# Optimization experiments

Measured on AMD Instinct MI355X. Metric: run time of the kernel, lower is better.

The kernel has to match this reference:

```python
import jax, jax.numpy as jnp
import numpy as np

DIM = 256
N_EMBED = 16384
BETA = 0.25
FIX_LEN = 30.0  # fix_len_l2norm


def setup_inputs() -> dict:
    key = jax.random.key(0)
    k1, k2 = jax.random.split(key)
    z = jax.random.normal(k1, (16, DIM, 32, 32), dtype=jnp.float32)
    embedding = jax.random.normal(k2, (N_EMBED, DIM), dtype=jnp.float32)
    return {"z": z, "embedding": embedding}


def reference(z, embedding):
    # pre_len_l2norm: mean over (b,h,w) of the channel-dim L2 norm of z [b,c,h,w]
    pre_len = jnp.mean(jnp.linalg.norm(z, axis=1))
    zt = jnp.transpose(z, (0, 2, 3, 1))  # b h w c
    # use_l2_norm=False path: rescale only if pre_len >= fix_len_l2norm
    scale = jnp.where(pre_len >= FIX_LEN, FIX_LEN / pre_len, 1.0)
    zt = zt * scale

    z_flat = zt.reshape(-1, DIM)  # [N_tok, dim]
    # norm_type != 'rela_llm' -> scaled_ratio = fix_len_l2norm
    zs = jax.lax.stop_gradient(z_flat) / FIX_LEN
    # squared L2 distance: |z|^2 + |e|^2 - 2 z.e   -> [N_tok, n_embed]
    d = (jnp.sum(zs * zs, axis=1, keepdims=True)
         + jnp.sum(embedding * embedding, axis=1)
         - 2.0 * jnp.einsum('bd,nd->bn', zs, embedding))
    idx = jnp.argmin(d, axis=1)  # [N_tok]

    z_q = embedding[idx].reshape(zt.shape) * FIX_LEN  # gather + rescale
    diff = BETA * jnp.mean((jax.lax.stop_gradient(z_q) - zt) ** 2)
    z_q = zt + jax.lax.stop_gradient(z_q - zt)  # straight-through
    z_q = jnp.transpose(z_q, (0, 3, 1, 2))  # b c h w
    return z_q, diff, idx
```

## Files before the change

### kernel.cpp

```cpp
#include <hip/hip_runtime.h>
#include <hip/hip_fp16.h>
#include <math.h>

#define FIXLEN 30.0f
#define BETA   0.25f

typedef unsigned short u16;
typedef unsigned int   u32;
typedef unsigned long long u64;
typedef _Float16 half8 __attribute__((ext_vector_type(8)));
typedef float    f32x4 __attribute__((ext_vector_type(4)));

#define NRM_OFF    0
#define NRMX_OFF   256
#define CST_OFF    512
#define CNT_OFF    576
#define DIFF_OFF   1024
#define ZMAX_OFF   2048
#define EMAXL_OFF  6144
#define EMAXE_OFF  14336
#define E2_OFF     22528
#define BESTN_OFF  88064
#define PCNT_OFF   153600
#define PLIST_OFF  219136
#define CIDX_OFF   743424
#define CE2_OFF    808960
#define LIST2_OFF  874496
#define E2MIN_OFF  940032
#define ZS_OFF     1048576
#define ZH_OFF     1792000
#define EHC_OFF    10180608

__device__ inline void gl_lds16(const void* g, void* l) {
    __builtin_amdgcn_global_load_lds(
        (const __attribute__((address_space(1))) unsigned int*)g,
        (__attribute__((address_space(3))) unsigned int*)l, 16, 0, 0);
}

__global__ void k_split_e(const float* __restrict__ emb, float* __restrict__ e2,
                          float* __restrict__ emaxl, float* __restrict__ emaxe,
                          float* __restrict__ e2minp) {
    int gidx = blockIdx.x * 256 + threadIdx.x;
    int n = gidx >> 5;
    int c8 = (gidx & 31) * 8;
    const float* ep = emb + (size_t)n * 256 + c8;
    float4 v0 = *(const float4*)ep;
    float4 v1 = *(const float4*)(ep + 4);
    float vv[8] = {v0.x, v0.y, v0.z, v0.w, v1.x, v1.y, v1.z, v1.w};
    float s2 = 0.f, r2 = 0.f;
    #pragma unroll
    for (int k = 0; k < 8; ++k) {
        __half h = __float2half(vv[k]);
        float r = vv[k] - __half2float(h);
        s2 = fmaf(vv[k], vv[k], s2);
        r2 = fmaf(r, r, r2);
    }
    #pragma unroll
    for (int off = 16; off > 0; off >>= 1) {
        s2 += __shfl_down(s2, off, 32);
        r2 += __shfl_down(r2, off, 32);
    }
    __shared__ float L1[8], L2[8];
    if ((threadIdx.x & 31) == 0) {
        e2[n] = s2;
        L1[threadIdx.x >> 5] = r2;
        L2[threadIdx.x >> 5] = s2;
    }
    __syncthreads();
    if (threadIdx.x == 0) {
        float a = 0.f, bmax = 0.f, bmin = 3.4e38f;
        #pragma unroll
        for (int i = 0; i < 8; ++i) {
            a = fmaxf(a, L1[i]);
            bmax = fmaxf(bmax, L2[i]);
            bmin = fminf(bmin, L2[i]);
        }
        emaxl[blockIdx.x] = a;
        emaxe[blockIdx.x] = bmax;
        e2minp[blockIdx.x] = bmin;
    }
}

__global__ void k_split_z(const float* __restrict__ z, u16* __restrict__ zh,
                          float* __restrict__ zmax_part, float* __restrict__ zsumP) {
    int bi = blockIdx.x;
    int b = bi >> 6, rest = bi & 63;
    int c0 = (rest >> 4) * 64, s0 = (rest & 15) * 64;
    __shared__ float ld[64][65];
    __shared__ float red2[64][4];
    __shared__ float redz[64][4];
    __shared__ float rmax[64];
    int tid = threadIdx.x;
    #pragma unroll
    for (int p = 0; p < 16; ++p) {
        int idx = p * 256 + tid;
        int cc = idx >> 6, ss = idx & 63;
        ld[cc][ss] = z[(size_t)b * 262144 + (size_t)(c0 + cc) * 1024 + s0 + ss];
    }
    __syncthreads();
    int ss2 = tid >> 2, cq = tid & 3;
    int t = b * 1024 + s0 + ss2;
    float r2 = 0.f, zacc = 0.f;
    u32 pk[8];
    #pragma unroll
    for (int k = 0; k < 8; ++k) pk[k] = 0;
    #pragma unroll
    for (int j = 0; j < 16; ++j) {
        float raw = ld[cq * 16 + j][ss2];
        zacc = fmaf(raw, raw, zacc);
        float v = raw * (1.0f / 30.0f);
        __half h = __float2half(v);
        float vh = __half2float(h);
        float r = v - vh;
        r2 = fmaf(r, r, r2);
        __half hs = __float2half(-2.0f * vh);
        pk[j >> 1] |= ((u32)__half_as_ushort(hs)) << ((j & 1) * 16);
    }
    u16* dst = zh + (size_t)t * 256 + c0 + cq * 16;
    *(uint4*)dst = make_uint4(pk[0], pk[1], pk[2], pk[3]);
    *(uint4*)(dst + 8) = make_uint4(pk[4], pk[5], pk[6], pk[7]);
    red2[ss2][cq] = r2;
    redz[ss2][cq] = zacc;
    __syncthreads();
    if (tid < 64) {
        rmax[tid] = red2[tid][0] + red2[tid][1] + red2[tid][2] + red2[tid][3];
        zsumP[(size_t)(rest >> 4) * 16384 + b * 1024 + s0 + tid] =
            redz[tid][0] + redz[tid][1] + redz[tid][2] + redz[tid][3];
    }
    __syncthreads();
    for (int off = 32; off > 0; off >>= 1) {
        if (tid < off) rmax[tid] = fmaxf(rmax[tid], rmax[tid + off]);
        __syncthreads();
    }
    if (tid == 0) zmax_part[bi] = rmax[0];
}

__global__ void k_norm2(const float* __restrict__ zsumP, float* __restrict__ nrm_part,
                        float* __restrict__ nrmx_part) {
    int t = blockIdx.x * 256 + threadIdx.x;
    float tot = zsumP[t] + zsumP[16384 + t] + zsumP[32768 + t] + zsumP[49152 + t];
    float nrm = sqrtf(tot);
    __shared__ float rs[256], rm[256];
    rs[threadIdx.x] = nrm; rm[threadIdx.x] = nrm;
    __syncthreads();
    for (int off = 128; off > 0; off >>= 1) {
        if (threadIdx.x < off) {
            rs[threadIdx.x] += rs[threadIdx.x + off];
            rm[threadIdx.x] = fmaxf(rm[threadIdx.x], rm[threadIdx.x + off]);
        }
        __syncthreads();
    }
    if (threadIdx.x == 0) { nrm_part[blockIdx.x] = rs[0]; nrmx_part[blockIdx.x] = rm[0]; }
}

__global__ void k_scalars(const float* __restrict__ nrm_part, const float* __restrict__ nrmx_part,
                          const float* __restrict__ zmax_part, const float* __restrict__ emaxl,
                          const float* __restrict__ emaxe, const float* __restrict__ e2minp,
                          float* __restrict__ cst, int* __restrict__ cnt) {
    int tid = threadIdx.x;
    float s = (tid < 64) ? nrm_part[tid] : 0.f;
    float m = (tid < 64) ? nrmx_part[tid] : 0.f;
    float zm = 0.f, el = 0.f, ee = 0.f, em = 3.4e38f;
    for (int i = tid; i < 1024; i += 256) zm = fmaxf(zm, zmax_part[i]);
    for (int i = tid; i < 2048; i += 256) {
        el = fmaxf(el, emaxl[i]);
        ee = fmaxf(ee, emaxe[i]);
        em = fminf(em, e2minp[i]);
    }
    __shared__ float S[256], M[256], Z[256], L[256], E[256], Q[256];
    S[tid] = s; M[tid] = m; Z[tid] = zm; L[tid] = el; E[tid] = ee; Q[tid] = em;
    __syncthreads();
    for (int off = 128; off > 0; off >>= 1) {
        if (tid < off) {
            S[tid] += S[tid + off];
            M[tid] = fmaxf(M[tid], M[tid + off]);
            Z[tid] = fmaxf(Z[tid], Z[tid + off]);
            L[tid] = fmaxf(L[tid], L[tid + off]);
            E[tid] = fmaxf(E[tid], E[tid + off]);
            Q[tid] = fminf(Q[tid], Q[tid + off]);
        }
        __syncthreads();
    }
    if (tid == 0) {
        float pre_len = S[0] * (1.0f / 16384.0f);
        float scale = (pre_len >= FIXLEN) ? (FIXLEN / pre_len) : 1.0f;
        float inv_s = 1.0f / scale;
        cst[0] = scale;
        cst[1] = inv_s;
        cst[3] = M[0];
        float maxA  = M[0] * (1.0f / 30.0f);
        float maxEl = sqrtf(L[0]);
        float maxE  = sqrtf(E[0]);
        float maxZl = 2.0f * sqrtf(Z[0]);
        float eps = 2.0f * (maxA * maxEl + maxZl * maxE + maxZl * maxEl) + 0.03f;
        float EPS2 = 2.0f * eps;
        cst[2] = EPS2;
        float e2min = Q[0];
        float T = fmaf(2.0f * maxA, sqrtf(e2min), e2min * inv_s);
        cst[4] = T + 2.0f * EPS2 + 1.0f;
        cnt[0] = 0;
        cnt[1] = 0;
    }
}

__global__ void k_select(const float* __restrict__ e2, const float* __restrict__ cst,
                         int* __restrict__ candIdx, int* __restrict__ cnt) {
    int n = blockIdx.x * 256 + threadIdx.x;
    float inv_s = cst[1], maxA = cst[3] * (1.0f / 30.0f), Tc = cst[4];
    float v = e2[n];
    float lb = fmaf(-2.0f * maxA, sqrtf(v), v * inv_s);
    bool sel = lb <= Tc;
    u64 mask = __ballot(sel);
    if (mask) {
        int lane = threadIdx.x & 63;
        int leader = __ffsll((long long)mask) - 1;
        int base = 0;
        if (lane == leader) base = atomicAdd(cnt + 1, __popcll(mask));
        base = __shfl(base, leader);
        if (sel) {
            int rank = __popcll(mask & ((1ull << lane) - 1ull));
            candIdx[base + rank] = n;
        }
    }
}

__global__ void k_gather(const float* __restrict__ emb, const float* __restrict__ e2,
                         const float* __restrict__ cst, const int* __restrict__ cnt,
                         const int* __restrict__ candIdx, u16* __restrict__ ehc,
                         float* __restrict__ ce2) {
    int w = threadIdx.x >> 6, lane = threadIdx.x & 63;
    int wid = blockIdx.x * 4 + w;
    int C = cnt[1];
    int NP = (C + 255) & ~255;
    float inv_s = cst[1];
    for (int slot = wid; slot < NP; slot += 256) {
        if (slot < C) {
            int n = candIdx[slot];
            float4 v = *(const float4*)&emb[(size_t)n * 256 + lane * 4];
            u32 p0 = (u32)__half_as_ushort(__float2half(v.x)) |
                     ((u32)__half_as_ushort(__float2half(v.y)) << 16);
            u32 p1 = (u32)__half_as_ushort(__float2half(v.z)) |
                     ((u32)__half_as_ushort(__float2half(v.w)) << 16);
            *(uint2*)&ehc[(size_t)slot * 256 + lane * 4] = make_uint2(p0, p1);
            if (lane == 0) ce2[slot] = e2[n] * inv_s;
        } else {
            *(uint2*)&ehc[(size_t)slot * 256 + lane * 4] = make_uint2(0u, 0u);
            if (lane == 0) ce2[slot] = 3.0e37f;
        }
    }
}

__launch_bounds__(256, 2)
__global__ void k_cmfma(const u16* __restrict__ zh, const u16* __restrict__ ehc,
                        const float* __restrict__ ce2, const float* __restrict__ cst,
                        int* __restrict__ cnt, const int* __restrict__ candIdx,
                        int* __restrict__ pcnt, int* __restrict__ plist,
                        int* __restrict__ list2, int* __restrict__ bestn) {
    __shared__ __align__(16) char lds[51200];
    char* sAb = lds;
    char* sB0 = lds + 16384;
    char* sB1 = lds + 32768;
    float* d1buf  = (float*)(lds + 49152);
    float* limitS = (float*)(lds + 49664);
    int*   pcnts  = (int*)(lds + 49792);
    int*   pls    = (int*)(lds + 49920);

    int t0 = blockIdx.x * 32;
    int C = cnt[1];
    int nch = (C + 255) >> 8;
    float THR = cst[2] + 0.0625f;
    int tid = threadIdx.x, w = tid >> 6, lane = tid & 63;
    int ml = lane & 15, q = lane >> 4;
    int wn0 = w * 64;
    int x7 = ml & 7;
    int xb = (ml >> 1) & 3;
    int slB = q ^ xb;

    #pragma unroll
    for (int i = 0; i < 4; ++i) {
        int el = i * 256 + tid;
        int row = el >> 5, j = el & 31;
        int jsrc = (j & 24) | ((j & 7) ^ (row & 7));
        gl_lds16(zh + (size_t)(t0 + row) * 256 + jsrc * 8, sAb + el * 16);
    }
    #pragma unroll
    for (int i = 0; i < 4; ++i) {
        int el = i * 256 + tid;
        int row = el >> 2, j = el & 3;
        int jsrc = j ^ ((row >> 1) & 3);
        gl_lds16(ehc + (size_t)row * 256 + jsrc * 8, sB0 + el * 16);
    }

    float b1[8];
    #pragma unroll
    for (int k = 0; k < 8; ++k) b1[k] = 3.4e38f;

    #pragma unroll 1
    for (int c = 0; c < nch; ++c) {
        float etb[4];
        #pragma unroll
        for (int tj = 0; tj < 4; ++tj) etb[tj] = ce2[c * 256 + wn0 + tj * 16 + ml];
        f32x4 acc[2][4];
        #pragma unroll
        for (int ti = 0; ti < 2; ++ti)
            #pragma unroll
            for (int tj = 0; tj < 4; ++tj)
                acc[ti][tj] = (f32x4){etb[tj], etb[tj], etb[tj], etb[tj]};
        #pragma unroll
        for (int s = 0; s < 8; ++s) {
            __syncthreads();
            if (s < 7 || c + 1 < nch) {
                int s2 = (s + 1) & 7;
                int cc2 = (s == 7) ? (c + 1) : c;
                char* dst = (s & 1) ? sB0 : sB1;
                #pragma unroll
                for (int i = 0; i < 4; ++i) {
                    int el = i * 256 + tid;
                    int row = el >> 2, j = el & 3;
                    int jsrc = j ^ ((row >> 1) & 3);
                    gl_lds16(ehc + (size_t)(cc2 * 256 + row) * 256 + s2 * 32 + jsrc * 8,
                             dst + el * 16);
                }
            }
            __builtin_amdgcn_sched_barrier(0);
            const char* sB = (s & 1) ? sB1 : sB0;
            half8 A[2], B[4];
            #pragma unroll
            for (int tj = 0; tj < 4; ++tj)
                B[tj] = *(const half8*)(sB + (wn0 + tj * 16 + ml) * 64 + slB * 16);
            int slotA = (s >> 1) * 8 + ((((s & 1) * 4) + q) ^ x7);
            #pragma unroll
            for (int ti = 0; ti < 2; ++ti)
                A[ti] = *(const half8*)(sAb + (ti * 16 + ml) * 512 + slotA * 16);
            #pragma unroll
            for (int ti = 0; ti < 2; ++ti)
                #pragma unroll
                for (int tj = 0; tj < 4; ++tj)
                    acc[ti][tj] = __builtin_amdgcn_mfma_f32_16x16x32_f16(A[ti], B[tj], acc[ti][tj], 0, 0, 0);
        }
        #pragma unroll
        for (int ti = 0; ti < 2; ++ti)
            #pragma unroll
            for (int r = 0; r < 4; ++r)
                #pragma unroll
                for (int tj = 0; tj < 4; ++tj)
                    b1[ti * 4 + r] = fminf(b1[ti * 4 + r], acc[ti][tj][r]);
    }

    #pragma unroll
    for (int k = 0; k < 8; ++k) {
        #pragma unroll
        for (int m = 1; m < 16; m <<= 1)
            b1[k] = fminf(b1[k], __shfl_xor(b1[k], m));
    }
    __syncthreads();
    if (ml == 0) {
        #pragma unroll
        for (int ti = 0; ti < 2; ++ti)
            #pragma unroll
            for (int r = 0; r < 4; ++r)
                d1buf[w * 32 + ti * 16 + q * 4 + r] = b1[ti * 4 + r];
    }
    __syncthreads();
    if (tid < 32) {
        float d = fminf(fminf(d1buf[tid], d1buf[32 + tid]),
                        fminf(d1buf[64 + tid], d1buf[96 + tid]));
        limitS[tid] = d + THR;
        pcnts[tid] = 0;
    }
    __syncthreads();
    float limit[8];
    #pragma unroll
    for (int ti = 0; ti < 2; ++ti)
        #pragma unroll
        for (int r = 0; r < 4; ++r)
            limit[ti * 4 + r] = limitS[ti * 16 + q * 4 + r];
    __syncthreads();

    #pragma unroll
    for (int i = 0; i < 4; ++i) {
        int el = i * 256 + tid;
        int row = el >> 2, j = el & 3;
        int jsrc = j ^ ((row >> 1) & 3);
        gl_lds16(ehc + (size_t)row * 256 + jsrc * 8, sB0 + el * 16);
    }
    #pragma unroll 1
    for (int c = 0; c < nch; ++c) {
        float etb[4];
        #pragma unroll
        for (int tj = 0; tj < 4; ++tj) etb[tj] = ce2[c * 256 + wn0 + tj * 16 + ml];
        f32x4 acc[2][4];
        #pragma unroll
        for (int ti = 0; ti < 2; ++ti)
            #pragma unroll
            for (int tj = 0; tj < 4; ++tj)
                acc[ti][tj] = (f32x4){etb[tj], etb[tj], etb[tj], etb[tj]};
        #pragma unroll
        for (int s = 0; s < 8; ++s) {
            __syncthreads();
            if (s < 7 || c + 1 < nch) {
                int s2 = (s + 1) & 7;
                int cc2 = (s == 7) ? (c + 1) : c;
                char* dst = (s & 1) ? sB0 : sB1;
                #pragma unroll
                for (int i = 0; i < 4; ++i) {
                    int el = i * 256 + tid;
                    int row = el >> 2, j = el & 3;
                    int jsrc = j ^ ((row >> 1) & 3);
                    gl_lds16(ehc + (size_t)(cc2 * 256 + row) * 256 + s2 * 32 + jsrc * 8,
                             dst + el * 16);
                }
            }
            __builtin_amdgcn_sched_barrier(0);
            const char* sB = (s & 1) ? sB1 : sB0;
            half8 A[2], B[4];
            #pragma unroll
            for (int tj = 0; tj < 4; ++tj)
                B[tj] = *(const half8*)(sB + (wn0 + tj * 16 + ml) * 64 + slB * 16);
            int slotA = (s >> 1) * 8 + ((((s & 1) * 4) + q) ^ x7);
            #pragma unroll
            for (int ti = 0; ti < 2; ++ti)
                A[ti] = *(const half8*)(sAb + (ti * 16 + ml) * 512 + slotA * 16);
            #pragma unroll
            for (int ti = 0; ti < 2; ++ti)
                #pragma unroll
                for (int tj = 0; tj < 4; ++tj)
                    acc[ti][tj] = __builtin_amdgcn_mfma_f32_16x16x32_f16(A[ti], B[tj], acc[ti][tj], 0, 0, 0);
        }
        int slot0 = c * 256 + wn0 + ml;
        #pragma unroll
        for (int ti = 0; ti < 2; ++ti) {
            #pragma unroll
            for (int r = 0; r < 4; ++r) {
                int k = ti * 4 + r;
                int row = ti * 16 + q * 4 + r;
                #pragma unroll
                for (int tj = 0; tj < 4; ++tj) {
                    if (acc[ti][tj][r] <= limit[k]) {
                        int pos = atomicAdd(&pcnts[row], 1);
                        if (pos < 8) pls[row * 8 + pos] = slot0 + tj * 16;
                    }
                }
            }
        }
    }
    __syncthreads();
    if (tid < 32) {
        int t = t0 + tid;
        int pc = pcnts[tid];
        if (pc == 1) {
            bestn[t] = candIdx[pls[tid * 8]];
        } else {
            int pos = atomicAdd(cnt, 1);
            list2[pos] = t;
            pcnt[t] = pc;
            int mm = pc < 8 ? pc : 8;
            for (int i = 0; i < mm; ++i) plist[t * 8 + i] = pls[tid * 8 + i];
        }
    }
}

__global__ void k_exact(const float* __restrict__ z, const float* __restrict__ emb,
                        const float* __restrict__ e2, const float* __restrict__ cst,
                        const int* __restrict__ cnt, const int* __restrict__ pcnt,
                        const int* __restrict__ plist, const int* __restrict__ candIdx,
                        const int* __restrict__ list2, int* __restrict__ bestn) {
    int w = threadIdx.x >> 6, lane = threadIdx.x & 63;
    int wid = blockIdx.x * 4 + w;
    int NQ = cnt[0], C = cnt[1];
    float inv_s = cst[1];
    for (int it = wid; it < NQ; it += 1024) {
        int t = list2[it];
        int b = t >> 10, hw = t & 1023;
        const float* zb = z + (size_t)b * 262144 + hw;
        float4 a4;
        a4.x = zb[(size_t)(lane * 4 + 0) << 10] * (1.0f / 30.0f);
        a4.y = zb[(size_t)(lane * 4 + 1) << 10] * (1.0f / 30.0f);
        a4.z = zb[(size_t)(lane * 4 + 2) << 10] * (1.0f / 30.0f);
        a4.w = zb[(size_t)(lane * 4 + 3) << 10] * (1.0f / 30.0f);
        int pc = pcnt[t];
        float bestv = 3.4e38f; int bi = 0x7fffffff;
        if (pc <= 8) {
            for (int i = 0; i < pc; ++i) {
                int n = candIdx[plist[t * 8 + i]];
                float4 e4 = *(const float4*)&emb[(size_t)n * 256 + lane * 4];
                float s = a4.x * e4.x + a4.y * e4.y + a4.z * e4.z + a4.w * e4.w;
                #pragma unroll
                for (int m = 1; m < 64; m <<= 1) s += __shfl_xor(s, m);
                float d = fmaf(-2.0f, s, e2[n] * inv_s);
                if (d < bestv || (d == bestv && n < bi)) { bestv = d; bi = n; }
            }
        } else {
            for (int slot = 0; slot < C; ++slot) {
                int n = candIdx[slot];
                float4 e4 = *(const float4*)&emb[(size_t)n * 256 + lane * 4];
                float s = a4.x * e4.x + a4.y * e4.y + a4.z * e4.z + a4.w * e4.w;
                #pragma unroll
                for (int m = 1; m < 64; m <<= 1) s += __shfl_xor(s, m);
                float d = fmaf(-2.0f, s, e2[n] * inv_s);
                if (d < bestv || (d == bestv && n < bi)) { bestv = d; bi = n; }
            }
        }
        if (lane == 0) bestn[t] = bi;
    }
}

__global__ void k_emit(const float* __restrict__ z, const float* __restrict__ emb,
                       const float* __restrict__ cst, const int* __restrict__ bestn,
                       float* __restrict__ out, float* __restrict__ diff_part) {
    int blk = blockIdx.x;
    int cq = blk >> 6, sub = blk & 63;
    int b = sub >> 2;
    int tl = (sub & 3) * 256 + threadIdx.x;
    int t = b * 1024 + tl;
    int bi = bestn[t];
    if (cq == 0) out[4194305 + t] = (float)bi;
    float scale = cst[0];
    const float* er = emb + (size_t)bi * 256 + cq * 64;
    const float* zr = z + (size_t)b * 262144 + (size_t)cq * 65536 + tl;
    float* orow = out + (size_t)b * 262144 + (size_t)cq * 65536 + tl;
    float ds = 0.f;
    #pragma unroll 8
    for (int j = 0; j < 64; ++j) {
        float qv = er[j] * FIXLEN;
        float zt = zr[(size_t)j << 10] * scale;
        float dd = qv - zt;
        ds = fmaf(dd, dd, ds);
        orow[(size_t)j << 10] = qv;
    }
    __shared__ float red[256];
    red[threadIdx.x] = ds;
    __syncthreads();
    for (int off = 128; off > 0; off >>= 1) {
        if (threadIdx.x < off) red[threadIdx.x] += red[threadIdx.x + off];
        __syncthreads();
    }
    if (threadIdx.x == 0) diff_part[blk] = red[0];
}

__global__ void k_diff(const float* __restrict__ diff_part, float* __restrict__ out) {
    int tid = threadIdx.x;
    __shared__ float red[256];
    red[tid] = diff_part[tid];
    __syncthreads();
    for (int off = 128; off > 0; off >>= 1) {
        if (tid < off) red[tid] += red[tid + off];
        __syncthreads();
    }
    if (tid == 0) out[4194304] = BETA * red[0] / 4194304.0f;
}

extern "C" void kernel_launch(void* const* d_in, const int* in_sizes, int n_in,
                              void* d_out, int out_size, void* d_ws, size_t ws_size,
                              hipStream_t stream) {
    const float* z   = (const float*)d_in[0];
    const float* emb = (const float*)d_in[1];
    float* out = (float*)d_out;
    char* wsb = (char*)d_ws;

    float* nrm_part  = (float*)(wsb + NRM_OFF);
    float* nrmx_part = (float*)(wsb + NRMX_OFF);
    float* cst       = (float*)(wsb + CST_OFF);
    int*   cnt       = (int*)(wsb + CNT_OFF);
    float* diff_part = (float*)(wsb + DIFF_OFF);
    float* zmax_part = (float*)(wsb + ZMAX_OFF);
    float* emaxl     = (float*)(wsb + EMAXL_OFF);
    float* emaxe     = (float*)(wsb + EMAXE_OFF);
    float* e2        = (float*)(wsb + E2_OFF);
    int*   bestn     = (int*)(wsb + BESTN_OFF);
    int*   pcnt      = (int*)(wsb + PCNT_OFF);
    int*   plist     = (int*)(wsb + PLIST_OFF);
    int*   candIdx   = (int*)(wsb + CIDX_OFF);
    float* ce2       = (float*)(wsb + CE2_OFF);
    int*   list2     = (int*)(wsb + LIST2_OFF);
    float* e2minp    = (float*)(wsb + E2MIN_OFF);
    float* zsumP     = (float*)(wsb + ZS_OFF);
    u16*   zh        = (u16*)(wsb + ZH_OFF);
    u16*   ehc       = (u16*)(wsb + EHC_OFF);

    k_split_e<<<2048, 256, 0, stream>>>(emb, e2, emaxl, emaxe, e2minp);
    k_split_z<<<1024, 256, 0, stream>>>(z, zh, zmax_part, zsumP);
    k_norm2<<<64, 256, 0, stream>>>(zsumP, nrm_part, nrmx_part);
    k_scalars<<<1, 256, 0, stream>>>(nrm_part, nrmx_part, zmax_part, emaxl, emaxe, e2minp, cst, cnt);
    k_select<<<64, 256, 0, stream>>>(e2, cst, candIdx, cnt);
    k_gather<<<64, 256, 0, stream>>>(emb, e2, cst, cnt, candIdx, ehc, ce2);
    k_cmfma<<<512, 256, 0, stream>>>(zh, ehc, ce2, cst, cnt, candIdx, pcnt, plist, list2, bestn);
    k_exact<<<256, 256, 0, stream>>>(z, emb, e2, cst, cnt, pcnt, plist, candIdx, list2, bestn);
    k_emit<<<256, 256, 0, stream>>>(z, emb, cst, bestn, out, diff_part);
    k_diff<<<1, 256, 0, stream>>>(diff_part, out);
}
```

Measured before the change: 157.0 us.

## Fuse small reduction, select and gather kernels using last-block atomics

Merges k_norm2 and k_scalars into one kernel, where the last block to finish, found through an atomic ticket, does the scalar reduction. It also fuses candidate selection with the fp16 gather of embeddings, and replaces the final k_diff kernel with an atomic float accumulation finalized by the last k_emit block. Counter and ce2 initialization move into k_split_e. The goal is to cut kernel launches and the small dependent passes between them. The trade-offs are non-deterministic float summation order for the diff value, and padded ehc slots that are no longer zeroed (their ce2 sentinel is set large instead).

```diff
diff --git a/kernel.cpp b/kernel.cpp
--- a/kernel.cpp
+++ b/kernel.cpp
@@ -15,7 +15,6 @@
 #define NRMX_OFF   256
 #define CST_OFF    512
 #define CNT_OFF    576
-#define DIFF_OFF   1024
 #define ZMAX_OFF   2048
 #define EMAXL_OFF  6144
 #define EMAXE_OFF  14336
@@ -39,10 +38,13 @@
 
 __global__ void k_split_e(const float* __restrict__ emb, float* __restrict__ e2,
                           float* __restrict__ emaxl, float* __restrict__ emaxe,
-                          float* __restrict__ e2minp) {
+                          float* __restrict__ e2minp, float* __restrict__ ce2,
+                          float* __restrict__ cst, int* __restrict__ cnt) {
     int gidx = blockIdx.x * 256 + threadIdx.x;
     int n = gidx >> 5;
     int c8 = (gidx & 31) * 8;
+    if (gidx == 0) { cnt[2] = 0; cnt[3] = 0; cst[6] = 0.f; }
+    if ((threadIdx.x & 31) == 0) ce2[n] = 3.0e37f;
     const float* ep = emb + (size_t)n * 256 + c8;
     float4 v0 = *(const float4*)ep;
     float4 v1 = *(const float4*)(ep + 4);
@@ -135,29 +137,35 @@
     if (tid == 0) zmax_part[bi] = rmax[0];
 }
 
-__global__ void k_norm2(const float* __restrict__ zsumP, float* __restrict__ nrm_part,
-                        float* __restrict__ nrmx_part) {
-    int t = blockIdx.x * 256 + threadIdx.x;
+__global__ void k_nscalars(const float* __restrict__ zsumP, const float* __restrict__ zmax_part,
+                           const float* __restrict__ emaxl, const float* __restrict__ emaxe,
+                           const float* __restrict__ e2minp, float* __restrict__ nrm_part,
+                           float* __restrict__ nrmx_part, float* __restrict__ cst,
+                           int* __restrict__ cnt) {
+    int tid = threadIdx.x;
+    int t = blockIdx.x * 256 + tid;
     float tot = zsumP[t] + zsumP[16384 + t] + zsumP[32768 + t] + zsumP[49152 + t];
     float nrm = sqrtf(tot);
     __shared__ float rs[256], rm[256];
-    rs[threadIdx.x] = nrm; rm[threadIdx.x] = nrm;
+    rs[tid] = nrm; rm[tid] = nrm;
     __syncthreads();
     for (int off = 128; off > 0; off >>= 1) {
-        if (threadIdx.x < off) {
-            rs[threadIdx.x] += rs[threadIdx.x + off];
-            rm[threadIdx.x] = fmaxf(rm[threadIdx.x], rm[threadIdx.x + off]);
+        if (tid < off) {
+            rs[tid] += rs[tid + off];
+            rm[tid] = fmaxf(rm[tid], rm[tid + off]);
         }
         __syncthreads();
     }
-    if (threadIdx.x == 0) { nrm_part[blockIdx.x] = rs[0]; nrmx_part[blockIdx.x] = rm[0]; }
-}
-
-__global__ void k_scalars(const float* __restrict__ nrm_part, const float* __restrict__ nrmx_part,
-                          const float* __restrict__ zmax_part, const float* __restrict__ emaxl,
-                          const float* __restrict__ emaxe, const float* __restrict__ e2minp,
-                          float* __restrict__ cst, int* __restrict__ cnt) {
-    int tid = threadIdx.x;
+    __shared__ int amLast;
+    if (tid == 0) {
+        nrm_part[blockIdx.x] = rs[0];
+        nrmx_part[blockIdx.x] = rm[0];
+        __threadfence();
+        amLast = (atomicAdd(&cnt[2], 1) == 63);
+    }
+    __syncthreads();
+    if (!amLast) return;
+    __threadfence();
     float s = (tid < 64) ? nrm_part[tid] : 0.f;
     float m = (tid < 64) ? nrmx_part[tid] : 0.f;
     float zm = 0.f, el = 0.f, ee = 0.f, em = 3.4e38f;
@@ -203,49 +211,48 @@
     }
 }
 
-__global__ void k_select(const float* __restrict__ e2, const float* __restrict__ cst,
-                         int* __restrict__ candIdx, int* __restrict__ cnt) {
-    int n = blockIdx.x * 256 + threadIdx.x;
+__global__ void k_selgather(const float* __restrict__ emb, const float* __restrict__ e2,
+                            const float* __restrict__ cst, int* __restrict__ candIdx,
+                            int* __restrict__ cnt, u16* __restrict__ ehc,
+                            float* __restrict__ ce2) {
+    __shared__ int localN[256];
+    __shared__ int lc, baseS;
+    int tid = threadIdx.x;
+    int n = blockIdx.x * 256 + tid;
+    if (tid == 0) lc = 0;
+    __syncthreads();
     float inv_s = cst[1], maxA = cst[3] * (1.0f / 30.0f), Tc = cst[4];
     float v = e2[n];
     float lb = fmaf(-2.0f * maxA, sqrtf(v), v * inv_s);
-    bool sel = lb <= Tc;
-    u64 mask = __ballot(sel);
-    if (mask) {
-        int lane = threadIdx.x & 63;
-        int leader = __ffsll((long long)mask) - 1;
-        int base = 0;
-        if (lane == leader) base = atomicAdd(cnt + 1, __popcll(mask));
-        base = __shfl(base, leader);
-        if (sel) {
-            int rank = __popcll(mask & ((1ull << lane) - 1ull));
-            candIdx[base + rank] = n;
-        }
-    }
-}
-
-__global__ void k_gather(const float* __restrict__ emb, const float* __restrict__ e2,
-                         const float* __restrict__ cst, const int* __restrict__ cnt,
-                         const int* __restrict__ candIdx, u16* __restrict__ ehc,
-                         float* __restrict__ ce2) {
-    int w = threadIdx.x >> 6, lane = threadIdx.x & 63;
-    int wid = blockIdx.x * 4 + w;
-    int C = cnt[1];
-    int NP = (C + 255) & ~255;
-    float inv_s = cst[1];
-    for (int slot = wid; slot < NP; slot += 256) {
-        if (slot < C) {
-            int n = candIdx[slot];
-            float4 v = *(const float4*)&emb[(size_t)n * 256 + lane * 4];
-            u32 p0 = (u32)__half_as_ushort(__float2half(v.x)) |
-                     ((u32)__half_as_ushort(__float2half(v.y)) << 16);
-            u32 p1 = (u32)__half_as_ushort(__float2half(v.z)) |
-                     ((u32)__half_as_ushort(__float2half(v.w)) << 16);
-            *(uint2*)&ehc[(size_t)slot * 256 + lane * 4] = make_uint2(p0, p1);
-            if (lane == 0) ce2[slot] = e2[n] * inv_s;
-        } else {
-            *(uint2*)&ehc[(size_t)slot * 256 + lane * 4] = make_uint2(0u, 0u);
-            if (lane == 0) ce2[slot] = 3.0e37f;
+    int myPos = -1;
+    if (lb <= Tc) myPos = atomicAdd(&lc, 1);
+    __syncthreads();
+    if (tid == 0) baseS = atomicAdd(cnt + 1, lc);
+    __syncthreads();
+    int L = lc, base = baseS;
+    if (myPos >= 0) {
+        localN[myPos] = n;
+        candIdx[base + myPos] = n;
+        ce2[base + myPos] = v * inv_s;
+    }
+    __syncthreads();
+    for (int i0 = 0; i0 < L; i0 += 8) {
+        int r = i0 + (tid >> 5);
+        if (r < L) {
+            int nn = localN[r];
+            int c8 = (tid & 31) * 8;
+            const float* ep = emb + (size_t)nn * 256 + c8;
+            float4 v0 = *(const float4*)ep;
+            float4 v1 = *(const float4*)(ep + 4);
+            u32 p0 = (u32)__half_as_ushort(__float2half(v0.x)) |
+                     ((u32)__half_as_ushort(__float2half(v0.y)) << 16);
+            u32 p1 = (u32)__half_as_ushort(__float2half(v0.z)) |
+                     ((u32)__half_as_ushort(__float2half(v0.w)) << 16);
+            u32 p2 = (u32)__half_as_ushort(__float2half(v1.x)) |
+                     ((u32)__half_as_ushort(__float2half(v1.y)) << 16);
+            u32 p3 = (u32)__half_as_ushort(__float2half(v1.z)) |
+                     ((u32)__half_as_ushort(__float2half(v1.w)) << 16);
+            *(uint4*)&ehc[(size_t)(base + r) * 256 + c8] = make_uint4(p0, p1, p2, p3);
         }
     }
 }
@@ -506,8 +513,8 @@
 }
 
 __global__ void k_emit(const float* __restrict__ z, const float* __restrict__ emb,
-                       const float* __restrict__ cst, const int* __restrict__ bestn,
-                       float* __restrict__ out, float* __restrict__ diff_part) {
+                       float* __restrict__ cst, const int* __restrict__ bestn,
+                       float* __restrict__ out, int* __restrict__ cnt) {
     int blk = blockIdx.x;
     int cq = blk >> 6, sub = blk & 63;
     int b = sub >> 2;
@@ -535,19 +542,16 @@
         if (threadIdx.x < off) red[threadIdx.x] += red[threadIdx.x + off];
         __syncthreads();
     }
-    if (threadIdx.x == 0) diff_part[blk] = red[0];
-}
-
-__global__ void k_diff(const float* __restrict__ diff_part, float* __restrict__ out) {
-    int tid = threadIdx.x;
-    __shared__ float red[256];
-    red[tid] = diff_part[tid];
-    __syncthreads();
-    for (int off = 128; off > 0; off >>= 1) {
-        if (tid < off) red[tid] += red[tid + off];
-        __syncthreads();
-    }
-    if (tid == 0) out[4194304] = BETA * red[0] / 4194304.0f;
+    if (threadIdx.x == 0) {
+        atomicAdd(&cst[6], red[0]);
+        __threadfence();
+        int tick = atomicAdd(&cnt[3], 1);
+        if (tick == 255) {
+            __threadfence();
+            float total = atomicAdd(&cst[6], 0.0f);
+            out[4194304] = BETA * total / 4194304.0f;
+        }
+    }
 }
 
 extern "C" void kernel_launch(void* const* d_in, const int* in_sizes, int n_in,
@@ -562,7 +566,6 @@
     float* nrmx_part = (float*)(wsb + NRMX_OFF);
     float* cst       = (float*)(wsb + CST_OFF);
     int*   cnt       = (int*)(wsb + CNT_OFF);
-    float* diff_part = (float*)(wsb + DIFF_OFF);
     float* zmax_part = (float*)(wsb + ZMAX_OFF);
     float* emaxl     = (float*)(wsb + EMAXL_OFF);
     float* emaxe     = (float*)(wsb + EMAXE_OFF);
@@ -578,14 +581,12 @@
     u16*   zh        = (u16*)(wsb + ZH_OFF);
     u16*   ehc       = (u16*)(wsb + EHC_OFF);
 
-    k_split_e<<<2048, 256, 0, stream>>>(emb, e2, emaxl, emaxe, e2minp);
+    k_split_e<<<2048, 256, 0, stream>>>(emb, e2, emaxl, emaxe, e2minp, ce2, cst, cnt);
     k_split_z<<<1024, 256, 0, stream>>>(z, zh, zmax_part, zsumP);
-    k_norm2<<<64, 256, 0, stream>>>(zsumP, nrm_part, nrmx_part);
-    k_scalars<<<1, 256, 0, stream>>>(nrm_part, nrmx_part, zmax_part, emaxl, emaxe, e2minp, cst, cnt);
-    k_select<<<64, 256, 0, stream>>>(e2, cst, candIdx, cnt);
-    k_gather<<<64, 256, 0, stream>>>(emb, e2, cst, cnt, candIdx, ehc, ce2);
+    k_nscalars<<<64, 256, 0, stream>>>(zsumP, zmax_part, emaxl, emaxe, e2minp,
+                                       nrm_part, nrmx_part, cst, cnt);
+    k_selgather<<<64, 256, 0, stream>>>(emb, e2, cst, candIdx, cnt, ehc, ce2);
     k_cmfma<<<512, 256, 0, stream>>>(zh, ehc, ce2, cst, cnt, candIdx, pcnt, plist, list2, bestn);
     k_exact<<<256, 256, 0, stream>>>(z, emb, e2, cst, cnt, pcnt, plist, candIdx, list2, bestn);
-    k_emit<<<256, 256, 0, stream>>>(z, emb, cst, bestn, out, diff_part);
-    k_diff<<<1, 256, 0, stream>>>(diff_part, out);
-}
+    k_emit<<<256, 256, 0, stream>>>(z, emb, cst, bestn, out, cnt);
+}
```

Result: no change. 156.4 us (-0.4%).
